# Performance work log

Hardware: AMD Instinct MI355X
Metric: run time of the kernel (lower is better)

The kernel has to match this reference:

```python
import jax, jax.numpy as jnp
import numpy as np

S, B, H, NH, M = 2048, 2, 2048, 16, 2048
D = H // NH
FF = 4 * H
NORM = float(np.sqrt(D))  # norm_factor = sqrt(head_dim), no layer scaling
MASK_FILL = jnp.float32(-1e4)


def _ln(x, g, b):
    mu = jnp.mean(x, -1, keepdims=True)
    var = jnp.mean(jnp.square(x - mu), -1, keepdims=True)
    return (x - mu) * jax.lax.rsqrt(var + 1e-5) * g + b


def _l2(x):  # F.normalize over last dim
    return x * jax.lax.rsqrt(jnp.sum(jnp.square(x), -1, keepdims=True) + 1e-12)


def _mlp(h, w1, b1, w2, b2):  # ParallelMLP: h -> 4h -> h with gelu
    return jax.nn.gelu(h @ w1 + b1) @ w2 + b2


def setup_inputs() -> dict:
    key = jax.random.key(0)
    ks = jax.random.split(key, 12)
    w = lambda k, sh: jax.random.normal(k, sh, jnp.float32) * 0.02
    return {
        'x': jax.random.normal(ks[0], (S, B, H), jnp.float32),
        'mem_hidden': jax.random.normal(ks[1], (M, B, H), jnp.float32),
        'mem_mask': jax.random.randint(ks[2], (B, 1, S, M), 0, 5) == 0,  # True = masked
        'ln1_g': jnp.ones((H,), jnp.float32), 'ln1_b': jnp.zeros((H,), jnp.float32),
        'ln2_g': jnp.ones((H,), jnp.float32), 'ln2_b': jnp.zeros((H,), jnp.float32),
        'ln3_g': jnp.ones((H,), jnp.float32), 'ln3_b': jnp.zeros((H,), jnp.float32),
        'w_mlp1_in': w(ks[3], (H, FF)), 'b_mlp1_in': jnp.zeros((FF,), jnp.float32),
        'w_mlp1_out': w(ks[4], (FF, H)), 'b_mlp1_out': jnp.zeros((H,), jnp.float32),
        'w_q': w(ks[5], (H, H)), 'b_q': jnp.zeros((H,), jnp.float32),
        'w_kv': w(ks[6], (H, 2 * H)), 'b_kv': jnp.zeros((2 * H,), jnp.float32),
        'w_dense': w(ks[7], (H, H)), 'b_dense': jnp.zeros((H,), jnp.float32),
        'w_mlp2_in': w(ks[8], (H, FF)), 'b_mlp2_in': jnp.zeros((FF,), jnp.float32),
        'w_mlp2_out': w(ks[9], (FF, H)), 'b_mlp2_out': jnp.zeros((H,), jnp.float32),
    }


def reference(x, mem_hidden, mem_mask, ln1_g, ln1_b, ln2_g, ln2_b, ln3_g, ln3_b,
              w_mlp1_in, b_mlp1_in, w_mlp1_out, b_mlp1_out,
              w_q, b_q, w_kv, b_kv, w_dense, b_dense,
              w_mlp2_in, b_mlp2_in, w_mlp2_out, b_mlp2_out):
    # NOTE: source literally replaces x with mlp1 output (no residual on mlp1)
    x = _mlp(_ln(x, ln1_g, ln1_b), w_mlp1_in, b_mlp1_in, w_mlp1_out, b_mlp1_out)

    # memory attention: l2-normalized query vs l2-normalized retrieved memory k/v
    h2 = _ln(x, ln2_g, ln2_b)
    q = _l2((h2 @ w_q + b_q).reshape(S, B, NH, D))              # [s,b,h,d]
    kv = (mem_hidden @ w_kv + b_kv).reshape(M, B, NH, 2 * D)    # hidden_to_kv
    k = _l2(kv[..., :D])                                        # [m,b,h,d]
    v = _l2(kv[..., D:])
    scores = jnp.einsum('sbhd,mbhd->bhsm', q, k) / NORM
    scores = jnp.where(mem_mask, MASK_FILL, scores)             # attention_mask_func fill
    probs = jax.nn.softmax(scores, axis=-1)
    ctx = jnp.einsum('bhsm,mbhd->sbhd', probs, v).reshape(S, B, H)
    x = x + ctx @ w_dense + b_dense                             # dense w/ skip_bias_add

    x = x + _mlp(_ln(x, ln3_g, ln3_b), w_mlp2_in, b_mlp2_in, w_mlp2_out, b_mlp2_out)
    return x
```

## Files before the change

### kernel.cpp

```cpp
#include <hip/hip_runtime.h>
#include <stdint.h>
#include <stddef.h>

typedef __attribute__((ext_vector_type(8))) short bf16x8;
typedef __attribute__((ext_vector_type(4))) float f32x4;
typedef unsigned short u16;
typedef unsigned int u32;
typedef unsigned long long u64;

static constexpr int S_ = 2048, B_ = 2, H_ = 2048, NH_ = 16, D_ = 128, M_ = 2048, FF_ = 8192;
static constexpr int SB_ = S_ * B_;
static constexpr int MB_ = M_ * B_;

__device__ __forceinline__ float b2f(u16 b) {
  union { u32 u; float f; } v; v.u = ((u32)b) << 16; return v.f;
}
__device__ __forceinline__ u16 f2b(float f) {
  union { float f; u32 u; } v; v.f = f;
  u32 u = v.u;
  return (u16)((u + 0x7FFFu + ((u >> 16) & 1u)) >> 16);
}
__device__ __forceinline__ float geluf(float x) {
  float x3 = x * x * x;
  return 0.5f * x * (1.0f + tanhf(0.7978845608028654f * (x + 0.044715f * x3)));
}

#define LDSP(p) (reinterpret_cast<__attribute__((address_space(3))) uint32_t*>(reinterpret_cast<uintptr_t>(p)))
#define GLBP(p) (reinterpret_cast<const __attribute__((address_space(1))) uint32_t*>(reinterpret_cast<uintptr_t>(p)))

__global__ void detect_kinds(const u32* __restrict__ x0, const u32* __restrict__ mask, int* __restrict__ flags) {
  if (threadIdx.x == 0 && blockIdx.x == 0) {
    int cnt = 0;
    for (int i = 0; i < 256; ++i) {
      u32 e = (x0[i] >> 7) & 0xFFu;
      if (e >= 118u && e <= 130u) ++cnt;
    }
    flags[0] = (cnt >= 128) ? 0 : 1;
    int all01 = 1, allf = 1, allb = 1;
    for (int i = 0; i < 256; ++i) {
      u32 v = mask[i];
      if (v > 1u) all01 = 0;
      if (v != 0u && v != 0x3F800000u) allf = 0;
      u32 lo = v & 0xFFFFu, hi = v >> 16;
      if ((lo != 0u && lo != 0x3F80u) || (hi != 0u && hi != 0x3F80u)) allb = 0;
    }
    flags[1] = all01 ? 1 : (allf ? 3 : (allb ? 2 : 0));
  }
}

__global__ void mask_bits(const void* __restrict__ mraw, const int* __restrict__ flags, u64* __restrict__ bm) {
  int i = blockIdx.x * 256 + threadIdx.x;
  int kind = flags[1];
  int masked;
  if (kind == 1)      masked = ((const int*)mraw)[i] != 0;
  else if (kind == 3) masked = ((const float*)mraw)[i] != 0.0f;
  else if (kind == 2) masked = ((const u16*)mraw)[i] != 0;
  else                masked = ((const unsigned char*)mraw)[i] != 0;
  u64 vote = __ballot(masked == 0);
  if ((threadIdx.x & 63) == 0) bm[i >> 6] = vote;
}

__global__ void cvt_all(const void* s0, const void* s1, const void* s2, const void* s3,
                        const void* s4, const void* s5, const void* s6, const void* s7,
                        const void* s8, const void* s9, const void* s10, const void* s11,
                        const void* s12, const int* __restrict__ flags, float* __restrict__ SM) {
  const int i = blockIdx.x * 256 + threadIdx.x;
  if (i >= 40960) return;
  const void* src; int off;
  if (i < 8192)       { src = s0;  off = 0; }
  else if (i < 10240) { src = s1;  off = 8192; }
  else if (i < 12288) { src = s2;  off = 10240; }
  else if (i < 16384) { src = s3;  off = 12288; }
  else if (i < 18432) { src = s4;  off = 16384; }
  else if (i < 26624) { src = s5;  off = 18432; }
  else if (i < 28672) { src = s6;  off = 26624; }
  else if (i < 30720) { src = s7;  off = 28672; }
  else if (i < 32768) { src = s8;  off = 30720; }
  else if (i < 34816) { src = s9;  off = 32768; }
  else if (i < 36864) { src = s10; off = 34816; }
  else if (i < 38912) { src = s11; off = 36864; }
  else                { src = s12; off = 38912; }
  const int j = i - off;
  SM[i] = flags[0] ? ((const float*)src)[j] : b2f(((const u16*)src)[j]);
}

__global__ void cast_in_bf16(const void* __restrict__ src, const int* __restrict__ flags, u16* __restrict__ dst, int n8) {
  int i = blockIdx.x * 256 + threadIdx.x;
  if (i >= n8) return;
  if (flags[0]) {
    const float4* p = (const float4*)src;
    float4 a = p[i * 2], c = p[i * 2 + 1];
    bf16x8 o;
    o[0] = (short)f2b(a.x); o[1] = (short)f2b(a.y); o[2] = (short)f2b(a.z); o[3] = (short)f2b(a.w);
    o[4] = (short)f2b(c.x); o[5] = (short)f2b(c.y); o[6] = (short)f2b(c.z); o[7] = (short)f2b(c.w);
    *(bf16x8*)&dst[i * 8] = o;
  } else {
    *(bf16x8*)&dst[i * 8] = ((const bf16x8*)src)[i];
  }
}

__global__ __launch_bounds__(256) void transpose_cast(const void* __restrict__ in, const int* __restrict__ flags,
                                                      u16* __restrict__ out, int R, int C) {
  __shared__ u16 tile[64][65];
  const int isf = flags[0];
  const int tr = blockIdx.y * 64, tc = blockIdx.x * 64;
  const int tx = threadIdx.x & 63, ty = threadIdx.x >> 6;
  const float* inf = (const float*)in;
  const u16* inb = (const u16*)in;
#pragma unroll
  for (int i = 0; i < 16; ++i) {
    int r = ty * 16 + i;
    size_t idx = (size_t)(tr + r) * C + tc + tx;
    tile[r][tx] = isf ? f2b(inf[idx]) : inb[idx];
  }
  __syncthreads();
#pragma unroll
  for (int i = 0; i < 16; ++i) {
    int c = ty * 16 + i;
    out[(size_t)(tc + c) * R + tr + tx] = tile[tx][c];
  }
}

template <int EXT>
__global__ __launch_bounds__(256) void layernorm_k(const void* __restrict__ xin, const int* __restrict__ flags,
                                                   const float* __restrict__ g, const float* __restrict__ bta,
                                                   u16* __restrict__ out) {
  const int row = blockIdx.x, t = threadIdx.x;
  float v[8];
  bool bfmode = EXT && (flags[0] == 0);
  if (bfmode) {
    const u16* xr = (const u16*)xin + (size_t)row * H_ + t * 8;
    bf16x8 a = *(const bf16x8*)xr;
#pragma unroll
    for (int j = 0; j < 8; ++j) v[j] = b2f((u16)a[j]);
  } else {
    const float* xr = (const float*)xin + (size_t)row * H_ + t * 8;
    float4 a = *(const float4*)xr, c = *(const float4*)(xr + 4);
    v[0] = a.x; v[1] = a.y; v[2] = a.z; v[3] = a.w;
    v[4] = c.x; v[5] = c.y; v[6] = c.z; v[7] = c.w;
  }
  float s1 = 0.f, s2 = 0.f;
#pragma unroll
  for (int j = 0; j < 8; ++j) { s1 += v[j]; s2 += v[j] * v[j]; }
#pragma unroll
  for (int off = 32; off > 0; off >>= 1) { s1 += __shfl_down(s1, off); s2 += __shfl_down(s2, off); }
  __shared__ float red[8];
  const int w = t >> 6;
  if ((t & 63) == 0) { red[w] = s1; red[4 + w] = s2; }
  __syncthreads();
  s1 = red[0] + red[1] + red[2] + red[3];
  s2 = red[4] + red[5] + red[6] + red[7];
  const float mean = s1 * (1.0f / H_);
  const float rstd = rsqrtf(s2 * (1.0f / H_) - mean * mean + 1e-5f);
  bf16x8 o;
#pragma unroll
  for (int j = 0; j < 8; ++j) {
    float y = (v[j] - mean) * rstd * g[t * 8 + j] + bta[t * 8 + j];
    o[j] = (short)f2b(y);
  }
  *(bf16x8*)(out + (size_t)row * H_ + t * 8) = o;
}

template <int GELU, int RES, int WF, int WB, int ODYN>
__global__ __launch_bounds__(256, 2) void gemmra(const u16* __restrict__ A, const u16* __restrict__ Bt,
                                                 const float* __restrict__ bias, const float* __restrict__ res,
                                                 void* __restrict__ outF, u16* __restrict__ outB,
                                                 const int* __restrict__ flags, int Mr, int N, int K) {
  __shared__ u16 lds[32768];
  const int t = threadIdx.x;
  const int w = t >> 6, l = t & 63, lr = l & 15, lk = l >> 4;
  const int wr = w >> 1, wc = w & 1;
  const int gx = gridDim.x, gy = gridDim.y;
  const int orig = blockIdx.y * gx + blockIdx.x;
  const int nwg = gx * gy, per = nwg >> 3;
  int tm, tn;
  if ((gx & 7) == 0 && (per & 7) == 0) {
    const int xcd = orig & 7, p = orig >> 3;
    const int ncx = gx >> 3, cy = per >> 3;
    const int ccol = xcd % ncx, crow = xcd / ncx;
    const int px = p & 7, py = p >> 3;
    tn = (ccol * 8 + px) * 128;
    tm = (crow * cy + py) * 128;
  } else {
    tn = (orig % gx) * 128;
    tm = (orig / gx) * 128;
  }
  u32 aofs[4], bofs[4];
#pragma unroll
  for (int i = 0; i < 4; ++i) {
    const int idx = i * 256 + t;
    const int srow = idx >> 3, sc = idx & 7;
    const int lc = sc ^ (srow & 7);
    aofs[i] = (u32)(tm + srow) * (u32)K + (u32)lc * 8;
    bofs[i] = (u32)(tn + srow) * (u32)K + (u32)lc * 8;
  }
  const int wdst = w * 512;
  const int cso0 = ((0 + lk) ^ (lr & 7)) * 8;
  const int cso1 = ((4 + lk) ^ (lr & 7)) * 8;
  int arow[4], brow[4];
#pragma unroll
  for (int f = 0; f < 4; ++f) {
    arow[f] = (wr * 64 + f * 16 + lr) * 64;
    brow[f] = (wc * 64 + f * 16 + lr) * 64;
  }

  const int NS = K >> 6;
  f32x4 acc[4][4] = {};

#define STG(sl) do {                                                                                  \
    u16* Ad = lds + ((sl) & 1) * 16384;                                                               \
    u16* Bd = Ad + 8192;                                                                              \
    const u32 ko = (u32)(sl) * 64;                                                                    \
    _Pragma("unroll")                                                                                 \
    for (int i = 0; i < 4; ++i) {                                                                     \
      __builtin_amdgcn_global_load_lds(GLBP(A + aofs[i] + ko), LDSP(Ad + i * 2048 + wdst), 16, 0, 0); \
      __builtin_amdgcn_global_load_lds(GLBP(Bt + bofs[i] + ko), LDSP(Bd + i * 2048 + wdst), 16, 0, 0);\
    }                                                                                                 \
  } while (0)
#define RD(afX, bqX, sl, cso) do {                                                                    \
    const u16* As_ = lds + ((sl) & 1) * 16384;                                                        \
    const u16* Bs_ = As_ + 8192;                                                                      \
    _Pragma("unroll")                                                                                 \
    for (int f = 0; f < 4; ++f) {                                                                     \
      afX[f] = *(const bf16x8*)(As_ + arow[f] + (cso));                                               \
      bqX[f] = *(const bf16x8*)(Bs_ + brow[f] + (cso));                                               \
    }                                                                                                 \
  } while (0)
#define MM(afX, bqX)                                                                                  \
  _Pragma("unroll") for (int nf = 0; nf < 4; ++nf)                                                    \
  _Pragma("unroll") for (int mf = 0; mf < 4; ++mf)                                                    \
    acc[mf][nf] = __builtin_amdgcn_mfma_f32_16x16x32_bf16(afX[mf], bqX[nf], acc[mf][nf], 0, 0, 0);

  bf16x8 afA[4], bqA[4], afB[4], bqB[4];

  STG(0);
  asm volatile("s_waitcnt vmcnt(0)" ::: "memory");
  __builtin_amdgcn_s_barrier();
  RD(afA, bqA, 0, cso0);
  asm volatile("s_waitcnt lgkmcnt(0)" ::: "memory");
  __builtin_amdgcn_sched_barrier(0);

  for (int s = 0; s < NS; ++s) {
    if (s + 1 < NS) STG(s + 1);
    RD(afB, bqB, s, cso1);
    __builtin_amdgcn_sched_barrier(0);
    __builtin_amdgcn_s_setprio(1);
    MM(afA, bqA);
    __builtin_amdgcn_s_setprio(0);
    asm volatile("s_waitcnt lgkmcnt(0)" ::: "memory");
    __builtin_amdgcn_sched_barrier(0);
    asm volatile("s_waitcnt vmcnt(0)" ::: "memory");
    __builtin_amdgcn_s_barrier();
    if (s + 1 < NS) RD(afA, bqA, s + 1, cso0);
    __builtin_amdgcn_sched_barrier(0);
    __builtin_amdgcn_s_setprio(1);
    MM(afB, bqB);
    __builtin_amdgcn_s_setprio(0);
    asm volatile("s_waitcnt lgkmcnt(0)" ::: "memory");
    __builtin_amdgcn_sched_barrier(0);
  }
#undef STG
#undef RD
#undef MM

  const int obf = ODYN ? (flags[0] ? 0 : 1) : 0;
  (void)Mr;
#pragma unroll
  for (int mf = 0; mf < 4; ++mf) {
#pragma unroll
    for (int nf = 0; nf < 4; ++nf) {
      const int col = tn + wc * 64 + nf * 16 + lr;
      const float bv = bias[col];
#pragma unroll
      for (int j = 0; j < 4; ++j) {
        const int rw = tm + wr * 64 + mf * 16 + lk * 4 + j;
        float vv = acc[mf][nf][j] + bv;
        if (RES) vv += res[(size_t)rw * N + col];
        if (GELU) vv = geluf(vv);
        if (WF) {
          if (ODYN && obf) ((u16*)outF)[(size_t)rw * N + col] = f2b(vv);
          else ((float*)outF)[(size_t)rw * N + col] = vv;
        }
        if (WB) outB[(size_t)rw * N + col] = f2b(vv);
      }
    }
  }
}

__global__ __launch_bounds__(256) void l2_q(const float* __restrict__ qpre, u16* __restrict__ Q) {
  const int t = threadIdx.x;
  const int g = blockIdx.x * 64 + (t >> 2);
  const int lg = t & 3;
  const int h = g & (NH_ - 1), sb = g >> 4;
  const float* p = qpre + (size_t)sb * H_ + h * D_ + lg * 32;
  float vv[32];
  float ss = 0.f;
#pragma unroll
  for (int i = 0; i < 8; ++i) {
    float4 a = *(const float4*)&p[i * 4];
    vv[i * 4 + 0] = a.x; vv[i * 4 + 1] = a.y; vv[i * 4 + 2] = a.z; vv[i * 4 + 3] = a.w;
    ss += a.x * a.x + a.y * a.y + a.z * a.z + a.w * a.w;
  }
  ss += __shfl_xor(ss, 1); ss += __shfl_xor(ss, 2);
  const float sc = rsqrtf(ss + 1e-12f);
  const int s = sb >> 1, b = sb & 1;
  u16* o = Q + ((size_t)(b * NH_ + h) * S_ + s) * D_ + lg * 32;
#pragma unroll
  for (int i = 0; i < 4; ++i) {
    bf16x8 ov;
#pragma unroll
    for (int j = 0; j < 8; ++j) ov[j] = (short)f2b(vv[i * 8 + j] * sc);
    *(bf16x8*)&o[i * 8] = ov;
  }
}

__global__ __launch_bounds__(256) void l2_kv(const float* __restrict__ kvpre, u16* __restrict__ Kq, u16* __restrict__ Vt) {
  __shared__ u16 vtT[128][72];
  const int t = threadIdx.x;
  const int bid = blockIdx.x;
  const int mt = bid & 31, h = (bid >> 5) & 15, b = bid >> 9;
  const int lm = t >> 2, lg = t & 3;
  const int m = mt * 64 + lm;
  const size_t rowoff = (size_t)(m * B_ + b) * (2 * H_) + h * 256;
  float vv[32];
  {
    const float* p = kvpre + rowoff + lg * 32;
    float ss = 0.f;
#pragma unroll
    for (int i = 0; i < 8; ++i) {
      float4 a = *(const float4*)&p[i * 4];
      vv[i * 4 + 0] = a.x; vv[i * 4 + 1] = a.y; vv[i * 4 + 2] = a.z; vv[i * 4 + 3] = a.w;
      ss += a.x * a.x + a.y * a.y + a.z * a.z + a.w * a.w;
    }
    ss += __shfl_xor(ss, 1); ss += __shfl_xor(ss, 2);
    const float sc = rsqrtf(ss + 1e-12f);
    u16* o = Kq + ((size_t)(b * NH_ + h) * M_ + m) * D_ + lg * 32;
#pragma unroll
    for (int i = 0; i < 4; ++i) {
      bf16x8 ov;
#pragma unroll
      for (int j = 0; j < 8; ++j) ov[j] = (short)f2b(vv[i * 8 + j] * sc);
      *(bf16x8*)&o[i * 8] = ov;
    }
  }
  {
    const float* p = kvpre + rowoff + 128 + lg * 32;
    float ss = 0.f;
#pragma unroll
    for (int i = 0; i < 8; ++i) {
      float4 a = *(const float4*)&p[i * 4];
      vv[i * 4 + 0] = a.x; vv[i * 4 + 1] = a.y; vv[i * 4 + 2] = a.z; vv[i * 4 + 3] = a.w;
      ss += a.x * a.x + a.y * a.y + a.z * a.z + a.w * a.w;
    }
    ss += __shfl_xor(ss, 1); ss += __shfl_xor(ss, 2);
    const float sc = rsqrtf(ss + 1e-12f);
#pragma unroll
    for (int i = 0; i < 32; ++i) vtT[lg * 32 + i][lm] = f2b(vv[i] * sc);
  }
  __syncthreads();
  const int d = t >> 1, half = t & 1;
  u16* o = Vt + ((size_t)(b * NH_ + h) * D_ + d) * M_ + mt * 64 + half * 32;
#pragma unroll
  for (int i = 0; i < 4; ++i) {
    bf16x8 ov = *(const bf16x8*)&vtT[d][half * 32 + i * 8];
    *(bf16x8*)&o[i * 8] = ov;
  }
}

__global__ __launch_bounds__(256, 3) void attn_k(const u16* __restrict__ Q, const u16* __restrict__ Kq,
                                                 const u16* __restrict__ Vt, const u32* __restrict__ BM32,
                                                 u16* __restrict__ ctx) {
  __shared__ u16 Kl[2][4096];
  __shared__ u16 Vl[2][4096];
  __shared__ u16 Pl[4][16 * 40];
  const int t = threadIdx.x, w = t >> 6, l = t & 63, lr = l & 15, lk = l >> 4;
  const int lin = blockIdx.x;
  const int xcd = lin & 7, idx = lin >> 3;
  const int bh = xcd * 4 + (idx >> 5);
  const int chunk = idx & 31;
  const int b = bh >> 4, h = bh & 15;
  const int srow = chunk * 64 + w * 16;
  const u16* Qb = Q + ((size_t)bh * S_ + srow) * D_;
  bf16x8 qf[4];
#pragma unroll
  for (int kc = 0; kc < 4; ++kc)
    qf[kc] = *(const bf16x8*)&Qb[lr * D_ + kc * 32 + lk * 8];
  f32x4 oacc[8] = {};
  float den[4] = {};
  const u16* Kb = Kq + (size_t)bh * M_ * D_;
  const u16* Vb = Vt + (size_t)bh * D_ * M_;
  const float invn = 0.08838834764831845f;
  u32 ksrc[2], vsrc[2];
#pragma unroll
  for (int i = 0; i < 2; ++i) {
    const int kidx = i * 256 + t;
    const int kr = kidx >> 4, kc_ = (kidx & 15) ^ (kr & 7);
    ksrc[i] = (u32)kr * D_ + (u32)kc_ * 8;
    const int vidx = i * 256 + t;
    const int vd = vidx >> 2, vc = (vidx & 3) ^ ((vd >> 1) & 3);
    vsrc[i] = (u32)vd * M_ + (u32)vc * 8;
  }
  const int wdst = w * 64 * 8;
  u32 mrow[4];
#pragma unroll
  for (int j2 = 0; j2 < 4; ++j2)
    mrow[j2] = ((u32)b * S_ + (u32)(srow + lk * 4 + j2)) * 64u;

#define STG(buf, m0) do {                                                                              \
    _Pragma("unroll")                                                                                  \
    for (int i = 0; i < 2; ++i) {                                                                      \
      __builtin_amdgcn_global_load_lds(GLBP(Kb + (size_t)(m0) * D_ + ksrc[i]),                         \
                                       LDSP(&Kl[buf][i * 2048 + wdst]), 16, 0, 0);                     \
      __builtin_amdgcn_global_load_lds(GLBP(Vb + (size_t)(m0) + vsrc[i]),                              \
                                       LDSP(&Vl[buf][i * 2048 + wdst]), 16, 0, 0);                     \
    }                                                                                                  \
  } while (0)

  STG(0, 0);
  asm volatile("s_waitcnt vmcnt(0)" ::: "memory");
  __builtin_amdgcn_s_barrier();
  int cur = 0;

  for (int t64 = 0; t64 < M_ / 32; ++t64) {
    const int m0 = t64 * 32;
    if (t64 + 1 < M_ / 32) STG(cur ^ 1, m0 + 32);
    u32 mw[4];
#pragma unroll
    for (int j2 = 0; j2 < 4; ++j2) mw[j2] = BM32[mrow[j2] + t64];
    f32x4 sc[2] = {};
#pragma unroll
    for (int mf = 0; mf < 2; ++mf) {
      const int r = mf * 16 + lr;
#pragma unroll
      for (int kc = 0; kc < 4; ++kc) {
        const int cc = ((kc * 4 + lk) ^ (r & 7));
        bf16x8 kfv = *(const bf16x8*)&Kl[cur][r * 128 + cc * 8];
        sc[mf] = __builtin_amdgcn_mfma_f32_16x16x32_bf16(qf[kc], kfv, sc[mf], 0, 0, 0);
      }
    }
#pragma unroll
    for (int j2 = 0; j2 < 4; ++j2) {
      const int rloc = lk * 4 + j2;
#pragma unroll
      for (int mf = 0; mf < 2; ++mf) {
        float p = __expf(sc[mf][j2] * invn);
        p = ((mw[j2] >> (mf * 16 + lr)) & 1u) ? p : 0.0f;
        den[j2] += p;
        Pl[w][rloc * 40 + mf * 16 + lr] = f2b(p);
      }
    }
    asm volatile("s_waitcnt lgkmcnt(0)" ::: "memory");
    __builtin_amdgcn_sched_barrier(0);
    bf16x8 pa = *(const bf16x8*)&Pl[w][lr * 40 + lk * 8];
#pragma unroll
    for (int nf = 0; nf < 8; ++nf) {
      const int d = nf * 16 + lr;
      const int cc = lk ^ ((d >> 1) & 3);
      bf16x8 vfv = *(const bf16x8*)&Vl[cur][d * 32 + cc * 8];
      oacc[nf] = __builtin_amdgcn_mfma_f32_16x16x32_bf16(pa, vfv, oacc[nf], 0, 0, 0);
    }
    asm volatile("s_waitcnt vmcnt(0)" ::: "memory");
    __builtin_amdgcn_s_barrier();
    cur ^= 1;
  }
#undef STG
#pragma unroll
  for (int j2 = 0; j2 < 4; ++j2) {
    float d = den[j2];
    d += __shfl_xor(d, 1); d += __shfl_xor(d, 2); d += __shfl_xor(d, 4); d += __shfl_xor(d, 8);
    den[j2] = 1.0f / fmaxf(d, 1e-20f);
  }
#pragma unroll
  for (int nf = 0; nf < 8; ++nf)
#pragma unroll
    for (int j2 = 0; j2 < 4; ++j2) {
      const int s = srow + lk * 4 + j2;
      const int dd = nf * 16 + lr;
      ctx[((size_t)s * B_ + b) * H_ + h * D_ + dd] = f2b(oacc[nf][j2] * den[j2]);
    }
}

extern "C" void kernel_launch(void* const* d_in, const int* in_sizes, int n_in,
                              void* d_out, int out_size, void* d_ws, size_t ws_size,
                              hipStream_t stream) {
  (void)in_sizes; (void)n_in; (void)out_size; (void)ws_size;
  char* ws = (char*)d_ws;
  u16* WT     = (u16*)(ws + 0);
  void* MID   = (void*)(ws + 33554432);
  float* XF   = (float*)(ws + 100663296);
  u16* HB     = (u16*)(ws + 134217728);
  u16* MEMB   = (u16*)(ws + 150994944);
  u16* QB     = (u16*)(ws + 167772160);
  u16* KB     = (u16*)(ws + 184549376);
  u16* VTB    = (u16*)(ws + 201326592);
  u64* BMB    = (u64*)(ws + 218103808);
  float* SM   = (float*)(ws + 234881024);
  int* FLAGS  = (int*)(ws + 235044864);

  float* Bias1  = SM + 0;
  float* Bias1o = SM + 8192;
  float* BiasQ  = SM + 10240;
  float* BiasKV = SM + 12288;
  float* BiasD  = SM + 16384;
  float* Bias2  = SM + 18432;
  float* Bias2o = SM + 26624;
  float* G1v = SM + 28672; float* B1v = SM + 30720;
  float* G2v = SM + 32768; float* B2v = SM + 34816;
  float* G3v = SM + 36864; float* B3v = SM + 38912;

  detect_kinds<<<1, 64, 0, stream>>>((const u32*)d_in[0], (const u32*)d_in[2], FLAGS);

  cvt_all<<<160, 256, 0, stream>>>(d_in[10], d_in[12], d_in[14], d_in[16], d_in[18],
                                   d_in[20], d_in[22], d_in[3], d_in[4], d_in[5],
                                   d_in[6], d_in[7], d_in[8], FLAGS, SM);

  mask_bits<<<(B_ * S_ * M_) / 256, 256, 0, stream>>>(d_in[2], FLAGS, BMB);
  cast_in_bf16<<<(MB_ * H_ / 8) / 256, 256, 0, stream>>>(d_in[1], FLAGS, MEMB, MB_ * H_ / 8);

  dim3 blk(256);
  layernorm_k<1><<<SB_, blk, 0, stream>>>(d_in[0], FLAGS, G1v, B1v, HB);
  transpose_cast<<<dim3(FF_ / 64, H_ / 64), blk, 0, stream>>>(d_in[9], FLAGS, WT, H_, FF_);
  gemmra<1, 0, 0, 1, 0><<<dim3(FF_ / 128, SB_ / 128), blk, 0, stream>>>(HB, WT, Bias1, nullptr, nullptr, (u16*)MID, FLAGS, SB_, FF_, H_);
  transpose_cast<<<dim3(H_ / 64, FF_ / 64), blk, 0, stream>>>(d_in[11], FLAGS, WT, FF_, H_);
  gemmra<0, 0, 1, 0, 0><<<dim3(H_ / 128, SB_ / 128), blk, 0, stream>>>((u16*)MID, WT, Bias1o, nullptr, XF, nullptr, FLAGS, SB_, H_, FF_);

  layernorm_k<0><<<SB_, blk, 0, stream>>>(XF, FLAGS, G2v, B2v, HB);
  transpose_cast<<<dim3(H_ / 64, H_ / 64), blk, 0, stream>>>(d_in[13], FLAGS, WT, H_, H_);
  gemmra<0, 0, 1, 0, 0><<<dim3(H_ / 128, SB_ / 128), blk, 0, stream>>>(HB, WT, BiasQ, nullptr, MID, nullptr, FLAGS, SB_, H_, H_);
  l2_q<<<(SB_ * NH_) / 64, blk, 0, stream>>>((const float*)MID, QB);
  transpose_cast<<<dim3(2 * H_ / 64, H_ / 64), blk, 0, stream>>>(d_in[15], FLAGS, WT, H_, 2 * H_);
  gemmra<0, 0, 1, 0, 0><<<dim3(2 * H_ / 128, MB_ / 128), blk, 0, stream>>>(MEMB, WT, BiasKV, nullptr, MID, nullptr, FLAGS, MB_, 2 * H_, H_);
  l2_kv<<<B_ * NH_ * (M_ / 64), blk, 0, stream>>>((const float*)MID, KB, VTB);
  attn_k<<<1024, blk, 0, stream>>>(QB, KB, VTB, (const u32*)BMB, MEMB);
  transpose_cast<<<dim3(H_ / 64, H_ / 64), blk, 0, stream>>>(d_in[17], FLAGS, WT, H_, H_);
  gemmra<0, 1, 1, 0, 0><<<dim3(H_ / 128, SB_ / 128), blk, 0, stream>>>(MEMB, WT, BiasD, XF, XF, nullptr, FLAGS, SB_, H_, H_);

  layernorm_k<0><<<SB_, blk, 0, stream>>>(XF, FLAGS, G3v, B3v, HB);
  transpose_cast<<<dim3(FF_ / 64, H_ / 64), blk, 0, stream>>>(d_in[19], FLAGS, WT, H_, FF_);
  gemmra<1, 0, 0, 1, 0><<<dim3(FF_ / 128, SB_ / 128), blk, 0, stream>>>(HB, WT, Bias2, nullptr, nullptr, (u16*)MID, FLAGS, SB_, FF_, H_);
  transpose_cast<<<dim3(H_ / 64, FF_ / 64), blk, 0, stream>>>(d_in[21], FLAGS, WT, FF_, H_);
  gemmra<0, 1, 1, 0, 1><<<dim3(H_ / 128, SB_ / 128), blk, 0, stream>>>((u16*)MID, WT, Bias2o, XF, d_out, nullptr, FLAGS, SB_, H_, FF_);
}
```

Measured before the change: 1.152 ms.

## Deepen GEMM LDS pipeline to four stages with K=32 slices

Restructures the bf16 GEMM main loop from a double-buffered K=64 scheme to a four-slot ring of K=32 slices, keeping two to three global-to-LDS loads in flight. It uses partial vmcnt waits instead of draining all loads each step, and a new swizzled LDS layout that packs two rows per 64-element line. The goal is to hide global memory latency better and cut full-drain stalls. In exchange there are twice as many barriers per K, and hand-tuned vmcnt counts that must match the number of in-flight loads.

```diff
diff --git a/kernel.cpp b/kernel.cpp
--- a/kernel.cpp
+++ b/kernel.cpp
@@ -185,79 +185,80 @@
     tn = (orig % gx) * 128;
     tm = (orig / gx) * 128;
   }
-  u32 aofs[4], bofs[4];
-#pragma unroll
-  for (int i = 0; i < 4; ++i) {
+  u32 aofs[2], bofs[2];
+#pragma unroll
+  for (int i = 0; i < 2; ++i) {
     const int idx = i * 256 + t;
-    const int srow = idx >> 3, sc = idx & 7;
-    const int lc = sc ^ (srow & 7);
-    aofs[i] = (u32)(tm + srow) * (u32)K + (u32)lc * 8;
-    bofs[i] = (u32)(tn + srow) * (u32)K + (u32)lc * 8;
+    const int sr = idx >> 3, sp = idx & 7;
+    const int spp = sp ^ (sr & 7);
+    const int row = (sr << 1) | (spp >> 2);
+    const int ck = spp & 3;
+    aofs[i] = (u32)(tm + row) * (u32)K + (u32)ck * 8;
+    bofs[i] = (u32)(tn + row) * (u32)K + (u32)ck * 8;
   }
   const int wdst = w * 512;
-  const int cso0 = ((0 + lk) ^ (lr & 7)) * 8;
-  const int cso1 = ((4 + lk) ^ (lr & 7)) * 8;
-  int arow[4], brow[4];
+  int offA[4], offB[4];
 #pragma unroll
   for (int f = 0; f < 4; ++f) {
-    arow[f] = (wr * 64 + f * 16 + lr) * 64;
-    brow[f] = (wc * 64 + f * 16 + lr) * 64;
-  }
-
-  const int NS = K >> 6;
+    const int Ra = wr * 64 + f * 16 + lr;
+    const int sra = Ra >> 1;
+    offA[f] = sra * 64 + (((((Ra & 1) << 2) | lk) ^ (sra & 7)) << 3);
+    const int Rb = wc * 64 + f * 16 + lr;
+    const int srb = Rb >> 1;
+    offB[f] = srb * 64 + (((((Rb & 1) << 2) | lk) ^ (srb & 7)) << 3);
+  }
+
+  const int NS = K >> 5;
   f32x4 acc[4][4] = {};
 
 #define STG(sl) do {                                                                                  \
-    u16* Ad = lds + ((sl) & 1) * 16384;                                                               \
-    u16* Bd = Ad + 8192;                                                                              \
-    const u32 ko = (u32)(sl) * 64;                                                                    \
+    u16* Ad = lds + ((sl) & 3) * 8192;                                                                \
+    u16* Bd = Ad + 4096;                                                                              \
+    const u32 ko = (u32)(sl) * 32;                                                                    \
     _Pragma("unroll")                                                                                 \
-    for (int i = 0; i < 4; ++i) {                                                                     \
+    for (int i = 0; i < 2; ++i) {                                                                     \
       __builtin_amdgcn_global_load_lds(GLBP(A + aofs[i] + ko), LDSP(Ad + i * 2048 + wdst), 16, 0, 0); \
       __builtin_amdgcn_global_load_lds(GLBP(Bt + bofs[i] + ko), LDSP(Bd + i * 2048 + wdst), 16, 0, 0);\
     }                                                                                                 \
   } while (0)
-#define RD(afX, bqX, sl, cso) do {                                                                    \
-    const u16* As_ = lds + ((sl) & 1) * 16384;                                                        \
-    const u16* Bs_ = As_ + 8192;                                                                      \
+#define RD(afX, bqX, sl) do {                                                                         \
+    const u16* As_ = lds + ((sl) & 3) * 8192;                                                         \
+    const u16* Bs_ = As_ + 4096;                                                                      \
     _Pragma("unroll")                                                                                 \
     for (int f = 0; f < 4; ++f) {                                                                     \
-      afX[f] = *(const bf16x8*)(As_ + arow[f] + (cso));                                               \
-      bqX[f] = *(const bf16x8*)(Bs_ + brow[f] + (cso));                                               \
+      afX[f] = *(const bf16x8*)(As_ + offA[f]);                                                       \
+      bqX[f] = *(const bf16x8*)(Bs_ + offB[f]);                                                       \
     }                                                                                                 \
   } while (0)
 #define MM(afX, bqX)                                                                                  \
+  __builtin_amdgcn_s_setprio(1);                                                                      \
   _Pragma("unroll") for (int nf = 0; nf < 4; ++nf)                                                    \
   _Pragma("unroll") for (int mf = 0; mf < 4; ++mf)                                                    \
-    acc[mf][nf] = __builtin_amdgcn_mfma_f32_16x16x32_bf16(afX[mf], bqX[nf], acc[mf][nf], 0, 0, 0);
-
-  bf16x8 afA[4], bqA[4], afB[4], bqB[4];
-
-  STG(0);
-  asm volatile("s_waitcnt vmcnt(0)" ::: "memory");
+    acc[mf][nf] = __builtin_amdgcn_mfma_f32_16x16x32_bf16(afX[mf], bqX[nf], acc[mf][nf], 0, 0, 0);    \
+  __builtin_amdgcn_s_setprio(0);
+
+  bf16x8 fAa[4], fAb[4], fBa[4], fBb[4];
+
+  STG(0); STG(1); STG(2);
+  asm volatile("s_waitcnt vmcnt(4)" ::: "memory");
   __builtin_amdgcn_s_barrier();
-  RD(afA, bqA, 0, cso0);
-  asm volatile("s_waitcnt lgkmcnt(0)" ::: "memory");
-  __builtin_amdgcn_sched_barrier(0);
-
-  for (int s = 0; s < NS; ++s) {
-    if (s + 1 < NS) STG(s + 1);
-    RD(afB, bqB, s, cso1);
-    __builtin_amdgcn_sched_barrier(0);
-    __builtin_amdgcn_s_setprio(1);
-    MM(afA, bqA);
-    __builtin_amdgcn_s_setprio(0);
-    asm volatile("s_waitcnt lgkmcnt(0)" ::: "memory");
-    __builtin_amdgcn_sched_barrier(0);
-    asm volatile("s_waitcnt vmcnt(0)" ::: "memory");
+  RD(fAa, fAb, 0);
+
+  for (int s = 0; s < NS; s += 2) {
+    if (s + 3 < NS) STG(s + 3);
+    RD(fBa, fBb, s + 1);
+    MM(fAa, fAb);
+    if (s + 3 < NS) { asm volatile("s_waitcnt vmcnt(4)" ::: "memory"); }
+    else            { asm volatile("s_waitcnt vmcnt(0)" ::: "memory"); }
     __builtin_amdgcn_s_barrier();
-    if (s + 1 < NS) RD(afA, bqA, s + 1, cso0);
-    __builtin_amdgcn_sched_barrier(0);
-    __builtin_amdgcn_s_setprio(1);
-    MM(afB, bqB);
-    __builtin_amdgcn_s_setprio(0);
-    asm volatile("s_waitcnt lgkmcnt(0)" ::: "memory");
-    __builtin_amdgcn_sched_barrier(0);
+    if (s + 4 < NS) STG(s + 4);
+    if (s + 2 < NS) RD(fAa, fAb, s + 2);
+    MM(fBa, fBb);
+    if (s + 2 < NS) {
+      if (s + 4 < NS) { asm volatile("s_waitcnt vmcnt(4)" ::: "memory"); }
+      else            { asm volatile("s_waitcnt vmcnt(0)" ::: "memory"); }
+      __builtin_amdgcn_s_barrier();
+    }
   }
 #undef STG
 #undef RD
```

Result: slower. 1.259 ms (+9.3%).

## Add 32x32x16 MFMA GEMM with XCD-aware tile mapping for FFN up-projections

Applied to the files above, without the earlier changes.

Adds a new bf16 GEMM kernel that uses 32x32x16 MFMA instructions in place of 16x16 ones. It double-buffers LDS through direct global-to-LDS loads with an XOR swizzle and interleaves LDS reads with MFMA issue. It also remaps workgroups so that neighbouring output tiles land on the same XCD, which should improve L2 reuse. Only the two 4H-wide FFN input GEMMs with GELU use it, aiming to cut their instruction and LDS-read overhead. The epilogue writes strided scalar values and the change depends on the new tile-to-lane mapping being correct.

```diff
diff --git a/kernel.cpp b/kernel.cpp
--- a/kernel.cpp
+++ b/kernel.cpp
@@ -4,6 +4,7 @@
 
 typedef __attribute__((ext_vector_type(8))) short bf16x8;
 typedef __attribute__((ext_vector_type(4))) float f32x4;
+typedef __attribute__((ext_vector_type(16))) float f32x16;
 typedef unsigned short u16;
 typedef unsigned int u32;
 typedef unsigned long long u64;
@@ -287,6 +288,137 @@
   }
 }
 
+template <int GELU, int RES, int WF, int WB, int ODYN>
+__global__ __launch_bounds__(256, 2) void g32ra(const u16* __restrict__ A, const u16* __restrict__ Bt,
+                                                const float* __restrict__ bias, const float* __restrict__ res,
+                                                void* __restrict__ outF, u16* __restrict__ outB,
+                                                const int* __restrict__ flags, int Mr, int N, int K) {
+  __shared__ u16 lds[32768];
+  const int t = threadIdx.x;
+  const int w = t >> 6, l = t & 63, lm = l & 31, lh = l >> 5;
+  const int wr = w >> 1, wc = w & 1;
+  const int gx = gridDim.x, gy = gridDim.y;
+  const int orig = blockIdx.y * gx + blockIdx.x;
+  const int nwg = gx * gy, per = nwg >> 3;
+  int tm, tn;
+  if ((gx & 7) == 0 && (per & 7) == 0) {
+    const int xcd = orig & 7, p = orig >> 3;
+    const int ncx = gx >> 3, cy = per >> 3;
+    const int ccol = xcd % ncx, crow = xcd / ncx;
+    const int px = p & 7, py = p >> 3;
+    tn = (ccol * 8 + px) * 128;
+    tm = (crow * cy + py) * 128;
+  } else {
+    tn = (orig % gx) * 128;
+    tm = (orig / gx) * 128;
+  }
+  u32 aofs[4], bofs[4];
+#pragma unroll
+  for (int i = 0; i < 4; ++i) {
+    const int idx = i * 256 + t;
+    const int srow = idx >> 3, sc = idx & 7;
+    const int lc = sc ^ ((srow >> 1) & 7);
+    aofs[i] = (u32)(tm + srow) * (u32)K + (u32)lc * 8;
+    bofs[i] = (u32)(tn + srow) * (u32)K + (u32)lc * 8;
+  }
+  const int wdst = w * 512;
+  int offA[2][4], offB[2][4];
+#pragma unroll
+  for (int mi = 0; mi < 2; ++mi)
+#pragma unroll
+    for (int ks = 0; ks < 4; ++ks) {
+      const int Ra = wr * 64 + mi * 32 + lm;
+      offA[mi][ks] = Ra * 64 + (((ks * 2 + lh) ^ ((Ra >> 1) & 7)) << 3);
+      const int Rb = wc * 64 + mi * 32 + lm;
+      offB[mi][ks] = Rb * 64 + (((ks * 2 + lh) ^ ((Rb >> 1) & 7)) << 3);
+    }
+
+  const int NS = K >> 6;
+  f32x16 acc[2][2] = {};
+
+#define STG(sl) do {                                                                                  \
+    u16* Ad = lds + ((sl) & 1) * 16384;                                                               \
+    u16* Bd = Ad + 8192;                                                                              \
+    const u32 ko = (u32)(sl) * 64;                                                                    \
+    _Pragma("unroll")                                                                                 \
+    for (int i = 0; i < 4; ++i) {                                                                     \
+      __builtin_amdgcn_global_load_lds(GLBP(A + aofs[i] + ko), LDSP(Ad + i * 2048 + wdst), 16, 0, 0); \
+      __builtin_amdgcn_global_load_lds(GLBP(Bt + bofs[i] + ko), LDSP(Bd + i * 2048 + wdst), 16, 0, 0);\
+    }                                                                                                 \
+  } while (0)
+#define RD(afX, bqX, sl, half) do {                                                                   \
+    const u16* As_ = lds + ((sl) & 1) * 16384;                                                        \
+    const u16* Bs_ = As_ + 8192;                                                                      \
+    _Pragma("unroll")                                                                                 \
+    for (int mi = 0; mi < 2; ++mi)                                                                    \
+    _Pragma("unroll")                                                                                 \
+      for (int k2 = 0; k2 < 2; ++k2) {                                                                \
+        afX[mi][k2] = *(const bf16x8*)(As_ + offA[mi][(half) * 2 + k2]);                              \
+        bqX[mi][k2] = *(const bf16x8*)(Bs_ + offB[mi][(half) * 2 + k2]);                              \
+      }                                                                                               \
+  } while (0)
+#define MM(afX, bqX)                                                                                  \
+  _Pragma("unroll") for (int k2 = 0; k2 < 2; ++k2)                                                    \
+  _Pragma("unroll") for (int mi = 0; mi < 2; ++mi)                                                    \
+  _Pragma("unroll") for (int ni = 0; ni < 2; ++ni)                                                    \
+    acc[mi][ni] = __builtin_amdgcn_mfma_f32_32x32x16_bf16(afX[mi][k2], bqX[ni][k2], acc[mi][ni], 0, 0, 0);
+
+  bf16x8 afA[2][2], bqA[2][2], afB[2][2], bqB[2][2];
+
+  STG(0);
+  asm volatile("s_waitcnt vmcnt(0)" ::: "memory");
+  __builtin_amdgcn_s_barrier();
+  RD(afA, bqA, 0, 0);
+  asm volatile("s_waitcnt lgkmcnt(0)" ::: "memory");
+  __builtin_amdgcn_sched_barrier(0);
+
+  for (int s = 0; s < NS; ++s) {
+    if (s + 1 < NS) STG(s + 1);
+    RD(afB, bqB, s, 1);
+    __builtin_amdgcn_sched_barrier(0);
+    __builtin_amdgcn_s_setprio(1);
+    MM(afA, bqA);
+    __builtin_amdgcn_s_setprio(0);
+    asm volatile("s_waitcnt lgkmcnt(0)" ::: "memory");
+    __builtin_amdgcn_sched_barrier(0);
+    asm volatile("s_waitcnt vmcnt(0)" ::: "memory");
+    __builtin_amdgcn_s_barrier();
+    if (s + 1 < NS) RD(afA, bqA, s + 1, 0);
+    __builtin_amdgcn_sched_barrier(0);
+    __builtin_amdgcn_s_setprio(1);
+    MM(afB, bqB);
+    __builtin_amdgcn_s_setprio(0);
+    asm volatile("s_waitcnt lgkmcnt(0)" ::: "memory");
+    __builtin_amdgcn_sched_barrier(0);
+  }
+#undef STG
+#undef RD
+#undef MM
+
+  const int obf = ODYN ? (flags[0] ? 0 : 1) : 0;
+  (void)Mr;
+#pragma unroll
+  for (int mi = 0; mi < 2; ++mi) {
+#pragma unroll
+    for (int ni = 0; ni < 2; ++ni) {
+      const int col = tn + wc * 64 + ni * 32 + lm;
+      const float bv = bias[col];
+#pragma unroll
+      for (int r = 0; r < 16; ++r) {
+        const int rw = tm + wr * 64 + mi * 32 + (r & 3) + 8 * (r >> 2) + 4 * lh;
+        float vv = acc[mi][ni][r] + bv;
+        if (RES) vv += res[(size_t)rw * N + col];
+        if (GELU) vv = geluf(vv);
+        if (WF) {
+          if (ODYN && obf) ((u16*)outF)[(size_t)rw * N + col] = f2b(vv);
+          else ((float*)outF)[(size_t)rw * N + col] = vv;
+        }
+        if (WB) outB[(size_t)rw * N + col] = f2b(vv);
+      }
+    }
+  }
+}
+
 __global__ __launch_bounds__(256) void l2_q(const float* __restrict__ qpre, u16* __restrict__ Q) {
   const int t = threadIdx.x;
   const int g = blockIdx.x * 64 + (t >> 2);
@@ -520,7 +652,7 @@
   dim3 blk(256);
   layernorm_k<1><<<SB_, blk, 0, stream>>>(d_in[0], FLAGS, G1v, B1v, HB);
   transpose_cast<<<dim3(FF_ / 64, H_ / 64), blk, 0, stream>>>(d_in[9], FLAGS, WT, H_, FF_);
-  gemmra<1, 0, 0, 1, 0><<<dim3(FF_ / 128, SB_ / 128), blk, 0, stream>>>(HB, WT, Bias1, nullptr, nullptr, (u16*)MID, FLAGS, SB_, FF_, H_);
+  g32ra<1, 0, 0, 1, 0><<<dim3(FF_ / 128, SB_ / 128), blk, 0, stream>>>(HB, WT, Bias1, nullptr, nullptr, (u16*)MID, FLAGS, SB_, FF_, H_);
   transpose_cast<<<dim3(H_ / 64, FF_ / 64), blk, 0, stream>>>(d_in[11], FLAGS, WT, FF_, H_);
   gemmra<0, 0, 1, 0, 0><<<dim3(H_ / 128, SB_ / 128), blk, 0, stream>>>((u16*)MID, WT, Bias1o, nullptr, XF, nullptr, FLAGS, SB_, H_, FF_);
 
@@ -537,7 +669,7 @@
 
   layernorm_k<0><<<SB_, blk, 0, stream>>>(XF, FLAGS, G3v, B3v, HB);
   transpose_cast<<<dim3(FF_ / 64, H_ / 64), blk, 0, stream>>>(d_in[19], FLAGS, WT, H_, FF_);
-  gemmra<1, 0, 0, 1, 0><<<dim3(FF_ / 128, SB_ / 128), blk, 0, stream>>>(HB, WT, Bias2, nullptr, nullptr, (u16*)MID, FLAGS, SB_, FF_, H_);
+  g32ra<1, 0, 0, 1, 0><<<dim3(FF_ / 128, SB_ / 128), blk, 0, stream>>>(HB, WT, Bias2, nullptr, nullptr, (u16*)MID, FLAGS, SB_, FF_, H_);
   transpose_cast<<<dim3(H_ / 64, FF_ / 64), blk, 0, stream>>>(d_in[21], FLAGS, WT, FF_, H_);
   gemmra<0, 1, 1, 0, 1><<<dim3(H_ / 128, SB_ / 128), blk, 0, stream>>>((u16*)MID, WT, Bias2o, XF, d_out, nullptr, FLAGS, SB_, H_, FF_);
 }
```

After: 1.173 ms. No clear change (+1.9%).
